# Kernel tuning notes

Measured on AMD Instinct MI355X. Metric: run time of the kernel, lower is better.

The kernel has to match this reference:

```python
import jax, jax.numpy as jnp
import numpy as np

NUM_HEADS = 16


def setup_inputs() -> dict:
    key = jax.random.key(0)
    kq, kk, kv = jax.random.split(key, 3)
    b, s, h = 1, 4096, 1024
    q = jax.random.normal(kq, (b, s, h), dtype=jnp.float32)
    k = jax.random.normal(kk, (b, s, h), dtype=jnp.float32)
    v = jax.random.normal(kv, (b, s, h), dtype=jnp.float32)
    return {"q": q, "k": k, "v": v}


def reference(q, k, v):
    b, s, hd = q.shape
    n = NUM_HEADS
    d = hd // n
    # b s (n d) -> b s n d
    qh = q.reshape(b, s, n, d)
    kh = k.reshape(b, s, n, d)
    vh = v.reshape(b, s, n, d)
    scale = 1.0 / jnp.sqrt(jnp.float32(d))
    # non-causal flash-attention math: softmax(qk^T * scale) v
    scores = jnp.einsum('bqnd,bknd->bnqk', qh, kh) * scale  # [b, n, s, s]
    probs = jax.nn.softmax(scores, axis=-1)
    out = jnp.einsum('bnqk,bknd->bqnd', probs, vh)  # [b, s, n, d]
    return out.reshape(b, s, hd)
```

## Files before the change

kernel.cpp:

```cpp
#include <hip/hip_runtime.h>

#define S_   4096
#define H_   1024
#define NH_  16
#define NT_  64
#define SCALE_LOG2E 0.18033688011112042f

typedef __attribute__((ext_vector_type(8)))  short short8;
typedef __attribute__((ext_vector_type(16))) float f32x16;

__device__ __forceinline__ unsigned short f2bf(float x) {
    union { float f; unsigned u; } c; c.f = x;
    unsigned r = c.u + 0x7fffu + ((c.u >> 16) & 1u);
    return (unsigned short)(r >> 16);
}
__device__ __forceinline__ unsigned pk2(float a, float b) {
    return (unsigned)f2bf(a) | ((unsigned)f2bf(b) << 16);
}
__device__ __forceinline__ unsigned pkt(float a, float b) {
    union { float f; unsigned u; } ca, cb; ca.f = a; cb.f = b;
    return __builtin_amdgcn_perm(cb.u, ca.u, 0x07060302u);
}

__global__ __launch_bounds__(256) void prepack(
    const float* __restrict__ k, const float* __restrict__ v,
    unsigned short* __restrict__ kp, unsigned short* __restrict__ vtp)
{
    __shared__ unsigned sK[64 * 33];
    __shared__ unsigned sV[64 * 33];

    const int t  = threadIdx.x;
    const int kt = blockIdx.x, hd = blockIdx.y;
    const size_t tb = ((size_t)hd * NT_ + kt) * 4096;
    uint4* gk = (uint4*)(kp + tb);
    uint4* gv = (uint4*)(vtp + tb);

    #pragma unroll
    for (int i = 0; i < 4; ++i) {
        int n   = t + 256 * i;
        int row = n >> 4, c4 = n & 15;
        size_t off = (size_t)(kt * 64 + row) * H_ + hd * 64 + c4 * 4;
        {
            float4 a = *(const float4*)(k + off);
            sK[row * 33 + c4 * 2]     = pk2(a.x, a.y);
            sK[row * 33 + c4 * 2 + 1] = pk2(a.z, a.w);
        }
        {
            float4 a = *(const float4*)(v + off);
            sV[row * 33 + c4 * 2]     = pk2(a.x, a.y);
            sV[row * 33 + c4 * 2 + 1] = pk2(a.z, a.w);
        }
    }
    __syncthreads();

    #pragma unroll
    for (int i = 0; i < 2; ++i) {
        int o = t + 256 * i;
        {
            int kc = o >> 6, key = o & 63;
            uint4 w;
            w.x = sK[key * 33 + kc * 4];
            w.y = sK[key * 33 + kc * 4 + 1];
            w.z = sK[key * 33 + kc * 4 + 2];
            w.w = sK[key * 33 + kc * 4 + 3];
            gk[o] = w;
        }
        {
            int kc = o >> 6, d = o & 63;
            int dp = d >> 1, sh = (d & 1) * 16;
            unsigned q[8];
            #pragma unroll
            for (int e = 0; e < 8; ++e)
                q[e] = (sV[(kc * 8 + e) * 33 + dp] >> sh) & 0xffffu;
            uint4 w;
            w.x = q[0] | (q[1] << 16);
            w.y = q[2] | (q[3] << 16);
            w.z = q[4] | (q[5] << 16);
            w.w = q[6] | (q[7] << 16);
            gv[o] = w;
        }
    }
}

__global__ __launch_bounds__(256, 2) void attn_main(
    const float* __restrict__ q,
    const unsigned short* __restrict__ kp,
    const unsigned short* __restrict__ vtp,
    float* __restrict__ out)
{
    __shared__ __align__(16) float sO[4 * 2048];
    __shared__ float sL[2 * 128];

    const int t   = threadIdx.x;
    const int b   = blockIdx.x;
    const int xcd = b & 7;
    const int bi  = b >> 3;
    const int hd  = xcd * 2 + (bi >> 5);
    const int qt  = bi & 31;

    const int w    = t >> 6;
    const int lane = t & 63;
    const int l31  = lane & 31;
    const int lhi  = lane >> 5;
    const int qg   = w >> 1;
    const int kh   = w & 1;

    const unsigned short* gK = kp  + (size_t)hd * NT_ * 4096;
    const unsigned short* gV = vtp + (size_t)hd * NT_ * 4096;

    short8 qf[2][4];
    #pragma unroll
    for (int s = 0; s < 2; ++s) {
        const float* qb = q + (size_t)(qt * 128 + qg * 64 + s * 32 + l31) * H_ + hd * 64 + lhi * 8;
        #pragma unroll
        for (int c = 0; c < 4; ++c) {
            float4 a  = *(const float4*)(qb + c * 16);
            float4 bb = *(const float4*)(qb + c * 16 + 4);
            union { short8 v; unsigned u[4]; } f;
            f.u[0] = pk2(a.x * SCALE_LOG2E, a.y * SCALE_LOG2E);
            f.u[1] = pk2(a.z * SCALE_LOG2E, a.w * SCALE_LOG2E);
            f.u[2] = pk2(bb.x * SCALE_LOG2E, bb.y * SCALE_LOG2E);
            f.u[3] = pk2(bb.z * SCALE_LOG2E, bb.w * SCALE_LOG2E);
            qf[s][c] = f.v;
        }
    }

    f32x16 Oacc[2][2];
    #pragma unroll
    for (int s = 0; s < 2; ++s)
        #pragma unroll
        for (int h = 0; h < 2; ++h)
            #pragma unroll
            for (int r = 0; r < 16; ++r) Oacc[s][h][r] = 0.0f;
    float2 ls[2];
    ls[0].x = 0.0f; ls[0].y = 0.0f; ls[1].x = 0.0f; ls[1].y = 0.0f;

    f32x16 zero16;
    #pragma unroll
    for (int r = 0; r < 16; ++r) zero16[r] = 0.0f;

    const int kOff = (kh * 32 + l31) * 8 + lhi * 512;
    const int vOff = l31 * 8 + (kh * 4 + lhi) * 512;
    const unsigned short* pK = gK + kOff;
    const unsigned short* pV = gV + vOff;

    short8 kfA[4], vfA[4], kfB[4], vfB[4];

#define LOADF(KF, VF, tile)                                                  \
    {                                                                        \
        const unsigned short* kt_ = pK + (size_t)(tile) * 4096;              \
        const unsigned short* vt_ = pV + (size_t)(tile) * 4096;              \
        KF[0] = *(const short8*)(kt_);                                       \
        KF[1] = *(const short8*)(kt_ + 1024);                                \
        KF[2] = *(const short8*)(kt_ + 2048);                                \
        KF[3] = *(const short8*)(kt_ + 3072);                                \
        VF[0] = *(const short8*)(vt_);                                       \
        VF[1] = *(const short8*)(vt_ + 256);                                 \
        VF[2] = *(const short8*)(vt_ + 1024);                                \
        VF[3] = *(const short8*)(vt_ + 1280);                                \
    }

#define SMAX(ST, LS, PU)                                                     \
    {                                                                        \
        _Pragma("unroll")                                                    \
        for (int i2_ = 0; i2_ < 8; ++i2_) {                                  \
            float p0 = __builtin_amdgcn_exp2f(ST[2 * i2_]);                  \
            float p1 = __builtin_amdgcn_exp2f(ST[2 * i2_ + 1]);              \
            LS.x += p0; LS.y += p1;                                          \
            PU[i2_] = pkt(p0, p1);                                           \
        }                                                                    \
    }

#define PVAC(PU, VF, OA)                                                     \
    {                                                                        \
        _Pragma("unroll")                                                    \
        for (int c_ = 0; c_ < 2; ++c_) {                                     \
            unsigned a0 = PU[4 * c_],     b0 = PU[4 * c_ + 2];               \
            unsigned a1 = PU[4 * c_ + 1], b1 = PU[4 * c_ + 3];               \
                                   \
            asm("v_permlane32_swap_b32 %0, %1" : "+v"(a0), "+v"(b0));        \
            asm("v_permlane32_swap_b32 %0, %1" : "+v"(a1), "+v"(b1));        \
            union { short8 v; unsigned u[4]; } pf;                           \
            pf.u[0] = a0; pf.u[1] = a1; pf.u[2] = b0; pf.u[3] = b1;          \
            OA[0] = __builtin_amdgcn_mfma_f32_32x32x16_bf16(pf.v, VF[2 * c_],     OA[0], 0, 0, 0); \
            OA[1] = __builtin_amdgcn_mfma_f32_32x32x16_bf16(pf.v, VF[2 * c_ + 1], OA[1], 0, 0, 0); \
        }                                                                    \
    }

#define COMPUTE(KF, VF)                                                      \
    {                                                                        \
              \
        f32x16 st0 = __builtin_amdgcn_mfma_f32_32x32x16_bf16(KF[0], qf[0][0], zero16, 0, 0, 0); \
        f32x16 st1 = __builtin_amdgcn_mfma_f32_32x32x16_bf16(KF[0], qf[1][0], zero16, 0, 0, 0); \
        st0 = __builtin_amdgcn_mfma_f32_32x32x16_bf16(KF[1], qf[0][1], st0, 0, 0, 0); \
        st1 = __builtin_amdgcn_mfma_f32_32x32x16_bf16(KF[1], qf[1][1], st1, 0, 0, 0); \
        st0 = __builtin_amdgcn_mfma_f32_32x32x16_bf16(KF[2], qf[0][2], st0, 0, 0, 0); \
        st1 = __builtin_amdgcn_mfma_f32_32x32x16_bf16(KF[2], qf[1][2], st1, 0, 0, 0); \
        st0 = __builtin_amdgcn_mfma_f32_32x32x16_bf16(KF[3], qf[0][3], st0, 0, 0, 0); \
        st1 = __builtin_amdgcn_mfma_f32_32x32x16_bf16(KF[3], qf[1][3], st1, 0, 0, 0); \
        unsigned pu0[8], pu1[8];                                             \
        SMAX(st0, ls[0], pu0);                                               \
        PVAC(pu0, VF, Oacc[0]);                                              \
        SMAX(st1, ls[1], pu1);                                               \
        PVAC(pu1, VF, Oacc[1]);                                              \
    }

    LOADF(kfA, vfA, 0);
    for (int kt2 = 0; kt2 < 31; ++kt2) {
        LOADF(kfB, vfB, 2 * kt2 + 1);
        COMPUTE(kfA, vfA);
        LOADF(kfA, vfA, 2 * kt2 + 2);
        COMPUTE(kfB, vfB);
    }
    LOADF(kfB, vfB, 63);
    COMPUTE(kfA, vfA);
    COMPUTE(kfB, vfB);

#undef LOADF
#undef SMAX
#undef PVAC
#undef COMPUTE

    #pragma unroll
    for (int s = 0; s < 2; ++s) {
        float lsum = ls[s].x + ls[s].y;
        lsum += __shfl_xor(lsum, 32);
        if (lhi == 0) sL[kh * 128 + qg * 64 + s * 32 + l31] = lsum;
    }
    if (kh == 1) {
        #pragma unroll
        for (int s = 0; s < 2; ++s) {
            float* o = sO + (qg * 2 + s) * 2048;
            #pragma unroll
            for (int h = 0; h < 2; ++h)
                #pragma unroll
                for (int r = 0; r < 16; ++r)
                    o[h * 1024 + r * 64 + lane] = Oacc[s][h][r];
        }
    }
    __syncthreads();
    if (kh == 0) {
        #pragma unroll
        for (int s = 0; s < 2; ++s) {
            float linv[4][4];
            #pragma unroll
            for (int qd = 0; qd < 4; ++qd) {
                int base = qg * 64 + s * 32 + 8 * qd + 4 * lhi;
                float4 a  = *(const float4*)(sL + base);
                float4 bb = *(const float4*)(sL + 128 + base);
                linv[qd][0] = __builtin_amdgcn_rcpf(a.x + bb.x);
                linv[qd][1] = __builtin_amdgcn_rcpf(a.y + bb.y);
                linv[qd][2] = __builtin_amdgcn_rcpf(a.z + bb.z);
                linv[qd][3] = __builtin_amdgcn_rcpf(a.w + bb.w);
            }
            const float* o = sO + (qg * 2 + s) * 2048;
            #pragma unroll
            for (int h = 0; h < 2; ++h)
                #pragma unroll
                for (int qd = 0; qd < 4; ++qd)
                    #pragma unroll
                    for (int e = 0; e < 4; ++e) {
                        int r   = 4 * qd + e;
                        int row = e + 8 * qd + 4 * lhi;
                        float val = (Oacc[s][h][r] + o[h * 1024 + r * 64 + lane]) * linv[qd][e];
                        out[(size_t)(qt * 128 + qg * 64 + s * 32 + row) * H_ + hd * 64 + h * 32 + l31] = val;
                    }
        }
    }
}

extern "C" void kernel_launch(void* const* d_in, const int* in_sizes, int n_in,
                              void* d_out, int out_size, void* d_ws, size_t ws_size,
                              hipStream_t stream) {
    const float* q = (const float*)d_in[0];
    const float* k = (const float*)d_in[1];
    const float* v = (const float*)d_in[2];
    float* out = (float*)d_out;

    unsigned short* kp  = (unsigned short*)d_ws;
    unsigned short* vtp = kp + (size_t)NH_ * NT_ * 4096;

    prepack<<<dim3(NT_, NH_), 256, 0, stream>>>(k, v, kp, vtp);
    attn_main<<<dim3(512), 256, 0, stream>>>(q, kp, vtp, out);
}
```

Baseline: 161.5 us.

## Stage K/V tiles through double-buffered LDS instead of direct per-wave global loads

```diff
diff --git a/kernel.cpp b/kernel.cpp
--- a/kernel.cpp
+++ b/kernel.cpp
@@ -88,6 +88,7 @@
     const unsigned short* __restrict__ vtp,
     float* __restrict__ out)
 {
+    __shared__ __align__(16) unsigned short sKV[2][8192];
     __shared__ __align__(16) float sO[4 * 2048];
     __shared__ float sL[2 * 128];
 
@@ -141,15 +142,30 @@
 
     const int kOff = (kh * 32 + l31) * 8 + lhi * 512;
     const int vOff = l31 * 8 + (kh * 4 + lhi) * 512;
-    const unsigned short* pK = gK + kOff;
-    const unsigned short* pV = gV + vOff;
-
-    short8 kfA[4], vfA[4], kfB[4], vfB[4];
-
-#define LOADF(KF, VF, tile)                                                  \
-    {                                                                        \
-        const unsigned short* kt_ = pK + (size_t)(tile) * 4096;              \
-        const unsigned short* vt_ = pV + (size_t)(tile) * 4096;              \
+
+#define STAGE_LOAD(RG, tile)                                                 \
+    {                                                                        \
+        const uint4* gk4 = (const uint4*)(gK + (size_t)(tile) * 4096);       \
+        const uint4* gv4 = (const uint4*)(gV + (size_t)(tile) * 4096);       \
+        RG[0] = gk4[t];                                                      \
+        RG[1] = gk4[t + 256];                                                \
+        RG[2] = gv4[t];                                                      \
+        RG[3] = gv4[t + 256];                                                \
+    }
+#define STAGE_WRITE(RG, buf)                                                 \
+    {                                                                        \
+        uint4* sk4 = (uint4*)(&sKV[buf][0]);                                 \
+        uint4* sv4 = (uint4*)(&sKV[buf][4096]);                              \
+        sk4[t]       = RG[0];                                                \
+        sk4[t + 256] = RG[1];                                                \
+        sv4[t]       = RG[2];                                                \
+        sv4[t + 256] = RG[3];                                                \
+    }
+
+#define LOADF_LDS(KF, VF, buf)                                               \
+    {                                                                        \
+        const unsigned short* kt_ = &sKV[buf][0] + kOff;                     \
+        const unsigned short* vt_ = &sKV[buf][4096] + vOff;                  \
         KF[0] = *(const short8*)(kt_);                                       \
         KF[1] = *(const short8*)(kt_ + 1024);                                \
         KF[2] = *(const short8*)(kt_ + 2048);                                \
@@ -177,7 +193,6 @@
         for (int c_ = 0; c_ < 2; ++c_) {                                     \
             unsigned a0 = PU[4 * c_],     b0 = PU[4 * c_ + 2];               \
             unsigned a1 = PU[4 * c_ + 1], b1 = PU[4 * c_ + 3];               \
-                                   \
             asm("v_permlane32_swap_b32 %0, %1" : "+v"(a0), "+v"(b0));        \
             asm("v_permlane32_swap_b32 %0, %1" : "+v"(a1), "+v"(b1));        \
             union { short8 v; unsigned u[4]; } pf;                           \
@@ -189,7 +204,6 @@
 
 #define COMPUTE(KF, VF)                                                      \
     {                                                                        \
-              \
         f32x16 st0 = __builtin_amdgcn_mfma_f32_32x32x16_bf16(KF[0], qf[0][0], zero16, 0, 0, 0); \
         f32x16 st1 = __builtin_amdgcn_mfma_f32_32x32x16_bf16(KF[0], qf[1][0], zero16, 0, 0, 0); \
         st0 = __builtin_amdgcn_mfma_f32_32x32x16_bf16(KF[1], qf[0][1], st0, 0, 0, 0); \
@@ -205,18 +219,23 @@
         PVAC(pu1, VF, Oacc[1]);                                              \
     }
 
-    LOADF(kfA, vfA, 0);
-    for (int kt2 = 0; kt2 < 31; ++kt2) {
-        LOADF(kfB, vfB, 2 * kt2 + 1);
-        COMPUTE(kfA, vfA);
-        LOADF(kfA, vfA, 2 * kt2 + 2);
-        COMPUTE(kfB, vfB);
-    }
-    LOADF(kfB, vfB, 63);
-    COMPUTE(kfA, vfA);
-    COMPUTE(kfB, vfB);
-
-#undef LOADF
+    uint4 rg[4];
+    STAGE_LOAD(rg, 0);
+    STAGE_WRITE(rg, 0);
+    __syncthreads();
+    for (int kt = 0; kt < NT_; ++kt) {
+        const int cur = kt & 1;
+        if (kt < NT_ - 1) STAGE_LOAD(rg, kt + 1);
+        short8 kf[4], vf[4];
+        LOADF_LDS(kf, vf, cur);
+        COMPUTE(kf, vf);
+        if (kt < NT_ - 1) STAGE_WRITE(rg, cur ^ 1);
+        __syncthreads();
+    }
+
+#undef STAGE_LOAD
+#undef STAGE_WRITE
+#undef LOADF_LDS
 #undef SMAX
 #undef PVAC
 #undef COMPUTE
```

New measurement: 163.8 us. Within noise of the previous version (+1.4%).
